# Optimization experiments

Measured on AMD Instinct MI355X. Metric: run time of the kernel, lower is better.

## Reference

```python
import jax, jax.numpy as jnp
import numpy as np

N_TOKENS = 16384
D_MODEL = 1024
N_EXPERTS = 4
TOP_K = 2
LN_EPS = 1e-6


def setup_inputs() -> dict:
    key = jax.random.key(0)
    ks = jax.random.split(key, 6)
    d, e = D_MODEL, N_EXPERTS
    return {
        "x": jax.random.normal(ks[0], (N_TOKENS, d), jnp.float32),
        "gate_w": jax.random.normal(ks[1], (e, d), jnp.float32) * (1.0 / np.sqrt(d)),
        "w1": jax.random.normal(ks[2], (e, 2 * d, d), jnp.float32) * (1.0 / np.sqrt(d)),
        "b1": jax.random.normal(ks[3], (e, 2 * d), jnp.float32) * 0.01,
        "w2": jax.random.normal(ks[4], (e, d, 2 * d), jnp.float32) * (1.0 / np.sqrt(2 * d)),
        "b2": jax.random.normal(ks[5], (e, d), jnp.float32) * 0.01,
        "gamma": jnp.ones((e, d), jnp.float32),
        "beta": jnp.zeros((e, d), jnp.float32),
    }


def _expert_ffn(x, w1e, b1e, w2e, b2e, ge, be):
    h = jax.nn.gelu(x @ w1e.T + b1e, approximate=False)   # [N, 2d]
    z = x + (h @ w2e.T + b2e)                              # residual, [N, d]
    mu = jnp.mean(z, axis=-1, keepdims=True)
    var = jnp.var(z, axis=-1, keepdims=True)
    return (z - mu) * jax.lax.rsqrt(var + LN_EPS) * ge + be


def reference(x, gate_w, w1, b1, w2, b2, gamma, beta):
    n = x.shape[0]
    scores = x @ gate_w.T                                  # [N, E]
    ew, ei = jax.lax.top_k(scores, TOP_K)                  # [N, K]
    ew = jax.nn.softmax(ew, axis=-1)
    # combine weights: dense [N, E] routing matrix (each row has K nonzeros)
    comb = jnp.zeros_like(scores).at[jnp.arange(n)[:, None], ei].add(ew)
    y = jnp.zeros_like(x)
    for e in range(N_EXPERTS):  # small fixed expert count
        y = y + comb[:, e:e + 1] * _expert_ffn(x, w1[e], b1[e], w2[e], b2[e], gamma[e], beta[e])
    return y
```

## Files before the change

kernel.cpp:

```cpp
#include <hip/hip_runtime.h>
#include <hip/hip_bf16.h>
#include <math.h>

#define NT 16384
#define DM 1024
#define NE 4

typedef __attribute__((ext_vector_type(8))) short short8;
typedef __attribute__((ext_vector_type(4))) float f32x4;

#define GLDS(g, l)                                                        \
  __builtin_amdgcn_global_load_lds(                                       \
      (const __attribute__((address_space(1))) void*)(g),                 \
      (__attribute__((address_space(3))) void*)(l), 16, 0, 0)

__device__ __forceinline__ float bf2f(short h) {
    union { unsigned u; float f; } v;
    v.u = ((unsigned)(unsigned short)h) << 16;
    return v.f;
}

__global__ __launch_bounds__(256) void detect_kernel(
    const unsigned int* __restrict__ xw, int* __restrict__ flag)
{
    __shared__ int red[4];
    const int t = threadIdx.x;
    int cnt = 0;
    #pragma unroll 4
    for (int i = 0; i < 64; ++i) {
        unsigned w = xw[t * 64 + i];
        unsigned e0 = (w >> 7) & 0xFFu;
        cnt += (e0 >= 100u && e0 <= 150u) ? 1 : 0;
    }
    #pragma unroll
    for (int o = 32; o > 0; o >>= 1) cnt += __shfl_xor(cnt, o);
    if ((t & 63) == 0) red[t >> 6] = cnt;
    __syncthreads();
    if (t == 0) {
        int tot = red[0] + red[1] + red[2] + red[3];
        *flag = (tot > 8192) ? 1 : 0;
    }
}

__global__ __launch_bounds__(256) void init_kernel(
    int* __restrict__ counts, int* __restrict__ idx)
{
    const int t = blockIdx.x * 256 + threadIdx.x;
    idx[t] = 0;
    if (t < NE) counts[t] = 0;
}

__global__ __launch_bounds__(256) void convert_big_kernel(
    const float* __restrict__ src, short* __restrict__ dst, int n,
    const int* __restrict__ flag)
{
    if (*flag) return;
    const int stride = gridDim.x * blockDim.x;
    const int t0 = blockIdx.x * blockDim.x + threadIdx.x;
    const float4* s = (const float4*)src;
    for (int i = t0; i < n / 4; i += stride) {
        float4 v = s[i];
        __hip_bfloat16 b0 = __float2bfloat16(v.x);
        __hip_bfloat16 b1 = __float2bfloat16(v.y);
        __hip_bfloat16 b2 = __float2bfloat16(v.z);
        __hip_bfloat16 b3 = __float2bfloat16(v.w);
        short4 o;
        o.x = *(short*)&b0; o.y = *(short*)&b1;
        o.z = *(short*)&b2; o.w = *(short*)&b3;
        *(short4*)(dst + (size_t)i * 4) = o;
    }
}

__global__ __launch_bounds__(256) void convert_small_kernel(
    const void* __restrict__ b1, const void* __restrict__ b2,
    const void* __restrict__ ga, const void* __restrict__ be,
    short* __restrict__ b1d, short* __restrict__ b2d,
    short* __restrict__ gad, short* __restrict__ bed,
    const int* __restrict__ flag)
{
    const int isbf = *flag;
    const int t = blockIdx.x * 256 + threadIdx.x;
    const void* src; short* dst; int i;
    if (t < 8192)      { src = b1; dst = b1d; i = t; }
    else if (t < 12288){ src = b2; dst = b2d; i = t - 8192; }
    else if (t < 16384){ src = ga; dst = gad; i = t - 12288; }
    else               { src = be; dst = bed; i = t - 16384; }
    short v;
    if (isbf) v = ((const short*)src)[i];
    else {
        __hip_bfloat16 b = __float2bfloat16(((const float*)src)[i]);
        v = *(short*)&b;
    }
    dst[i] = v;
}

__global__ __launch_bounds__(256) void gate_kernel(
    const void* __restrict__ x, const void* __restrict__ gw,
    float* __restrict__ comb, int* __restrict__ choice,
    const int* __restrict__ flag)
{
    const int lane  = threadIdx.x & 63;
    const int token = blockIdx.x * 4 + (threadIdx.x >> 6);
    double s0 = 0., s1 = 0., s2 = 0., s3 = 0.;
    if (*flag) {
        const short8* xr = (const short8*)((const short*)x + (size_t)token * DM);
        const short8* g0 = (const short8*)((const short*)gw + 0 * DM);
        const short8* g1 = (const short8*)((const short*)gw + 1 * DM);
        const short8* g2 = (const short8*)((const short*)gw + 2 * DM);
        const short8* g3 = (const short8*)((const short*)gw + 3 * DM);
        #pragma unroll
        for (int c = 0; c < 2; ++c) {
            short8 xv = xr[c * 64 + lane];
            short8 a0 = g0[c * 64 + lane], a1 = g1[c * 64 + lane];
            short8 a2 = g2[c * 64 + lane], a3 = g3[c * 64 + lane];
            #pragma unroll
            for (int j = 0; j < 8; ++j) {
                double xd = (double)bf2f(xv[j]);
                s0 += xd * (double)bf2f(a0[j]);
                s1 += xd * (double)bf2f(a1[j]);
                s2 += xd * (double)bf2f(a2[j]);
                s3 += xd * (double)bf2f(a3[j]);
            }
        }
    } else {
        const float4* xr = (const float4*)((const float*)x + (size_t)token * DM);
        const float4* g0 = (const float4*)((const float*)gw + 0 * DM);
        const float4* g1 = (const float4*)((const float*)gw + 1 * DM);
        const float4* g2 = (const float4*)((const float*)gw + 2 * DM);
        const float4* g3 = (const float4*)((const float*)gw + 3 * DM);
        #pragma unroll
        for (int c = 0; c < 4; ++c) {
            float4 xv = xr[c * 64 + lane];
            float4 a0 = g0[c * 64 + lane], a1 = g1[c * 64 + lane];
            float4 a2 = g2[c * 64 + lane], a3 = g3[c * 64 + lane];
            s0 += (double)xv.x * a0.x + (double)xv.y * a0.y + (double)xv.z * a0.z + (double)xv.w * a0.w;
            s1 += (double)xv.x * a1.x + (double)xv.y * a1.y + (double)xv.z * a1.z + (double)xv.w * a1.w;
            s2 += (double)xv.x * a2.x + (double)xv.y * a2.y + (double)xv.z * a2.z + (double)xv.w * a2.w;
            s3 += (double)xv.x * a3.x + (double)xv.y * a3.y + (double)xv.z * a3.z + (double)xv.w * a3.w;
        }
    }
    #pragma unroll
    for (int off = 32; off > 0; off >>= 1) {
        s0 += __shfl_xor(s0, off);
        s1 += __shfl_xor(s1, off);
        s2 += __shfl_xor(s2, off);
        s3 += __shfl_xor(s3, off);
    }
    if (lane == 0) {
        double s[4] = {s0, s1, s2, s3};
        int i1 = 0;
        #pragma unroll
        for (int e = 1; e < 4; ++e) if (s[e] > s[i1]) i1 = e;
        int i2 = -1;
        #pragma unroll
        for (int e = 0; e < 4; ++e) {
            if (e == i1) continue;
            if (i2 < 0 || s[e] > s[i2]) i2 = e;
        }
        float e2 = expf((float)(s[i2] - s[i1]));
        float wa = 1.0f / (1.0f + e2);
        float wb = e2 * wa;
        float* cr = comb + (size_t)token * 4;
        #pragma unroll
        for (int e = 0; e < 4; ++e)
            cr[e] = (e == i1) ? wa : ((e == i2) ? wb : 0.0f);
        choice[token] = i1 | (i2 << 8);
    }
}

__global__ __launch_bounds__(256) void route_kernel(
    const int* __restrict__ choice, int* __restrict__ counts,
    int* __restrict__ idx, int* __restrict__ pos)
{
    __shared__ int T[4][8];
    __shared__ int base[4];
    const int tid = threadIdx.x, w = tid >> 6, lane = tid & 63;
    const int t = blockIdx.x * 256 + tid;
    const int c = choice[t];
    const int e0 = c & 0xFF, e1 = (c >> 8) & 0xFF;
    const unsigned long long lt = ((unsigned long long)1 << lane) - 1;
    int rank0 = 0, rank1 = 0;
    #pragma unroll
    for (int e = 0; e < 4; ++e) {
        unsigned long long m0 = __ballot(e0 == e);
        unsigned long long m1 = __ballot(e1 == e);
        if (e0 == e) rank0 = __popcll(m0 & lt);
        if (e1 == e) rank1 = __popcll(m1 & lt);
        if (lane == 0) { T[w][e] = __popcll(m0); T[w][4 + e] = __popcll(m1); }
    }
    __syncthreads();
    if (tid < 4) {
        int tot = 0;
        #pragma unroll
        for (int w2 = 0; w2 < 4; ++w2) tot += T[w2][tid] + T[w2][4 + tid];
        base[tid] = atomicAdd(&counts[tid], tot);
    }
    __syncthreads();
    int off0 = base[e0], off1 = base[e1];
    #pragma unroll
    for (int w2 = 0; w2 < 4; ++w2) {
        if (w2 < w) off0 += T[w2][e0];
        off1 += T[w2][e1];
        if (w2 < w) off1 += T[w2][4 + e1];
    }
    const int p0 = off0 + rank0;
    const int p1 = off1 + rank1;
    idx[e0 * NT + p0] = t;
    idx[e1 * NT + p1] = t;
    pos[t] = p0 | (p1 << 16);
}

template <int EPI, int BM, int BN>
__global__ __launch_bounds__(512, 2) void gemm256(
    const short* __restrict__ Araw, const short* __restrict__ Acvt,
    const short* __restrict__ Braw, const short* __restrict__ Bcvt,
    const short* __restrict__ biasAll,
    void* __restrict__ Cout,
    const int* __restrict__ idxAll,
    const int* __restrict__ counts,
    int c0, int N, int K, const int* __restrict__ flag,
    int eArg, int Rarg)
{
    constexpr int WM = 2, WN = 4;
    constexpr int WTM = BM / WM;
    constexpr int WTN = BN / WN;
    constexpr int MT  = WTM / 16;
    constexpr int NTt = WTN / 16;
    constexpr int ACH = BM / 64;
    constexpr int BCH = BN / 64;
    constexpr int NLD = ACH + BCH;

    const int e    = (Rarg < 0) ? eArg : (int)blockIdx.z;
    const int cnt  = counts[e] - c0;
    const int rowc = (int)blockIdx.y * BM;
    if (rowc >= cnt) return;

    int hRow0 = 0, zRow0 = 0;
    if (Rarg >= 0) {
        hRow0 = e * Rarg;
        int pre = 0;
        #pragma unroll
        for (int i = 0; i < NE; ++i) pre += (i < e) ? counts[i] : 0;
        zRow0 = pre + c0;
    }

    const short* A = (*flag) ? Araw : Acvt;
    const short* B = ((*flag) ? Braw : Bcvt) + (size_t)e * 2 * DM * DM;
    const short* bias = biasAll + (size_t)e * N;

    __shared__ __align__(16) short sA[2][BM * 64];
    __shared__ __align__(16) short sB[2][BN * 64];

    const int tid  = threadIdx.x;
    const int wid  = tid >> 6;
    const int col0 = (int)blockIdx.x * BN;
    const int wm = wid >> 2, wn = wid & 3;
    const int quad = (tid & 63) >> 4;
    const int mrow = tid & 15;

    const int scol = (((tid & 7) ^ ((tid >> 3) & 7)) * 8);
    const short* gA[ACH];
    const short* gB[BCH];
    #pragma unroll
    for (int i = 0; i < ACH; ++i) {
        const int lr = i * 64 + (tid >> 3);
        size_t grow;
        if (EPI == 0) grow = (size_t)idxAll[(size_t)e * NT + c0 + rowc + lr];
        else          grow = (size_t)(hRow0 + rowc + lr);
        gA[i] = A + grow * (size_t)K + scol;
    }
    #pragma unroll
    for (int j = 0; j < BCH; ++j)
        gB[j] = B + (size_t)(col0 + j * 64 + (tid >> 3)) * K + scol;

    f32x4 acc[MT][NTt];
    #pragma unroll
    for (int m = 0; m < MT; ++m)
        #pragma unroll
        for (int n = 0; n < NTt; ++n)
            acc[m][n] = (f32x4){0.f, 0.f, 0.f, 0.f};

    auto stage = [&](int buf, int k0) {
        short* dA = &sA[buf][0] + wid * 512;
        short* dB = &sB[buf][0] + wid * 512;
        #pragma unroll
        for (int i = 0; i < ACH; ++i) GLDS(gA[i] + k0, dA + i * 4096);
        #pragma unroll
        for (int j = 0; j < BCH; ++j) GLDS(gB[j] + k0, dB + j * 4096);
    };

    const int swz  = (mrow & 7) << 4;
    const int boff = (quad * 16) ^ swz;

    const int ntiles = K / 64;
    stage(0, 0);
    int cur = 0;
    for (int t = 0; t < ntiles; ++t) {
        if (t + 1 < ntiles) {
            stage(cur ^ 1, (t + 1) * 64);
            if (NLD == 8)
                asm volatile("s_waitcnt vmcnt(8)" ::: "memory");
            else
                asm volatile("s_waitcnt vmcnt(6)" ::: "memory");
        } else {
            asm volatile("s_waitcnt vmcnt(0)" ::: "memory");
        }
        __builtin_amdgcn_s_barrier();
        __builtin_amdgcn_sched_barrier(0);
        const char* sAc = (const char*)&sA[cur][0];
        const char* sBc = (const char*)&sB[cur][0];
        #pragma unroll
        for (int kk = 0; kk < 64; kk += 32) {
            const int kb = (kk * 2) ^ boff;
            short8 a[MT], b[NTt];
            #pragma unroll
            for (int m = 0; m < MT; ++m) {
                const int R = wm * WTM + m * 16 + mrow;
                a[m] = *(const short8*)(sAc + R * 128 + kb);
            }
            #pragma unroll
            for (int n = 0; n < NTt; ++n) {
                const int R = wn * WTN + n * 16 + mrow;
                b[n] = *(const short8*)(sBc + R * 128 + kb);
            }
            #pragma unroll
            for (int m = 0; m < MT; ++m)
                #pragma unroll
                for (int n = 0; n < NTt; ++n)
                    acc[m][n] = __builtin_amdgcn_mfma_f32_16x16x32_bf16(
                        a[m], b[n], acc[m][n], 0, 0, 0);
        }
        asm volatile("s_waitcnt lgkmcnt(0)" ::: "memory");
        __builtin_amdgcn_sched_barrier(0);
        __builtin_amdgcn_s_barrier();
        cur ^= 1;
    }

    #pragma unroll
    for (int m = 0; m < MT; ++m) {
        #pragma unroll
        for (int n = 0; n < NTt; ++n) {
            const int col = col0 + wn * WTN + n * 16 + mrow;
            const float bval = bf2f(bias[col]);
            #pragma unroll
            for (int i = 0; i < 4; ++i) {
                const int lrow = rowc + wm * WTM + m * 16 + quad * 4 + i;
                if (lrow < cnt) {
                    float v = acc[m][n][i] + bval;
                    if (EPI == 0) {
                        v = 0.5f * v * (1.0f + erff(v * 0.70710678118654752f));
                        ((__hip_bfloat16*)Cout)[(size_t)(hRow0 + lrow) * N + col] =
                            __float2bfloat16(v);
                    } else {
                        ((float*)Cout)[(size_t)(zRow0 + lrow) * N + col] = v;
                    }
                }
            }
        }
    }
}

__global__ __launch_bounds__(256) void ln_fused_kernel(
    const float* __restrict__ z,
    const void* __restrict__ xraw,
    const float* __restrict__ comb,
    const int* __restrict__ choice,
    const int* __restrict__ pos,
    const short* __restrict__ gammaAll,
    const short* __restrict__ betaAll,
    void* __restrict__ y,
    const int* __restrict__ counts, const int* __restrict__ flag)
{
    const int isbf = *flag;
    const int lane = threadIdx.x & 63;
    const int t = blockIdx.x * 4 + (threadIdx.x >> 6);

    const int ca = counts[0], cb = counts[1], cc = counts[2];
    const int ch = choice[t];
    const int e0 = ch & 0xFF, e1 = (ch >> 8) & 0xFF;
    const int pp = pos[t];
    const int p0 = pp & 0xFFFF, p1 = (pp >> 16) & 0xFFFF;
    const int b0r = (e0 > 0 ? ca : 0) + (e0 > 1 ? cb : 0) + (e0 > 2 ? cc : 0);
    const int b1r = (e1 > 0 ? ca : 0) + (e1 > 1 ? cb : 0) + (e1 > 2 ? cc : 0);
    const float w0 = comb[(size_t)t * 4 + e0];
    const float w1 = comb[(size_t)t * 4 + e1];

    const f32x4* z0r = (const f32x4*)(z + (size_t)(b0r + p0) * DM);
    const f32x4* z1r = (const f32x4*)(z + (size_t)(b1r + p1) * DM);

    f32x4 v0[4], v1[4];
    float s0 = 0.f, q0 = 0.f, s1 = 0.f, q1 = 0.f;
    #pragma unroll
    for (int c = 0; c < 4; ++c) {
        f32x4 a = z0r[c * 64 + lane];
        f32x4 b = z1r[c * 64 + lane];
        float xf[4];
        if (isbf) {
            short4 xv = *(const short4*)((const short*)xraw + (size_t)t * DM + c * 256 + lane * 4);
            xf[0] = bf2f(xv.x); xf[1] = bf2f(xv.y); xf[2] = bf2f(xv.z); xf[3] = bf2f(xv.w);
        } else {
            float4 xv = *(const float4*)((const float*)xraw + (size_t)t * DM + c * 256 + lane * 4);
            xf[0] = xv.x; xf[1] = xv.y; xf[2] = xv.z; xf[3] = xv.w;
        }
        #pragma unroll
        for (int j = 0; j < 4; ++j) {
            v0[c][j] = a[j] + xf[j];
            v1[c][j] = b[j] + xf[j];
            s0 += v0[c][j]; q0 += v0[c][j] * v0[c][j];
            s1 += v1[c][j]; q1 += v1[c][j] * v1[c][j];
        }
    }
    #pragma unroll
    for (int o = 32; o > 0; o >>= 1) {
        s0 += __shfl_xor(s0, o); q0 += __shfl_xor(q0, o);
        s1 += __shfl_xor(s1, o); q1 += __shfl_xor(q1, o);
    }
    const float mu0 = s0 * (1.0f / DM);
    const float r0  = rsqrtf(fmaxf(q0 * (1.0f / DM) - mu0 * mu0, 0.0f) + 1e-6f);
    const float mu1 = s1 * (1.0f / DM);
    const float r1  = rsqrtf(fmaxf(q1 * (1.0f / DM) - mu1 * mu1, 0.0f) + 1e-6f);

    #pragma unroll
    for (int c = 0; c < 4; ++c) {
        const int id = c * 256 + lane * 4;
        short4 g0v  = *(const short4*)(gammaAll + (size_t)e0 * DM + id);
        short4 be0v = *(const short4*)(betaAll  + (size_t)e0 * DM + id);
        short4 g1v  = *(const short4*)(gammaAll + (size_t)e1 * DM + id);
        short4 be1v = *(const short4*)(betaAll  + (size_t)e1 * DM + id);
        const float g0f[4]  = {bf2f(g0v.x),  bf2f(g0v.y),  bf2f(g0v.z),  bf2f(g0v.w)};
        const float b0f[4]  = {bf2f(be0v.x), bf2f(be0v.y), bf2f(be0v.z), bf2f(be0v.w)};
        const float g1f[4]  = {bf2f(g1v.x),  bf2f(g1v.y),  bf2f(g1v.z),  bf2f(g1v.w)};
        const float b1f[4]  = {bf2f(be1v.x), bf2f(be1v.y), bf2f(be1v.z), bf2f(be1v.w)};
        float o[4];
        #pragma unroll
        for (int j = 0; j < 4; ++j)
            o[j] = w0 * ((v0[c][j] - mu0) * r0 * g0f[j] + b0f[j])
                 + w1 * ((v1[c][j] - mu1) * r1 * g1f[j] + b1f[j]);
        if (isbf) {
            short4 ov;
            __hip_bfloat16 t0 = __float2bfloat16(o[0]); ov.x = *(short*)&t0;
            __hip_bfloat16 t1 = __float2bfloat16(o[1]); ov.y = *(short*)&t1;
            __hip_bfloat16 t2 = __float2bfloat16(o[2]); ov.z = *(short*)&t2;
            __hip_bfloat16 t3 = __float2bfloat16(o[3]); ov.w = *(short*)&t3;
            *(short4*)((short*)y + (size_t)t * DM + id) = ov;
        } else {
            float4 ov = {o[0], o[1], o[2], o[3]};
            *(float4*)((float*)y + (size_t)t * DM + id) = ov;
        }
    }
}

__global__ __launch_bounds__(256) void ln_kernel(
    const float* __restrict__ z, const void* __restrict__ xraw,
    const float* __restrict__ comb, const int* __restrict__ choice,
    const __hip_bfloat16* __restrict__ gamma,
    const __hip_bfloat16* __restrict__ beta,
    void* __restrict__ y, const int* __restrict__ idxl,
    const int* __restrict__ count, int c0,
    int expert, const int* __restrict__ flag)
{
    const int isbf = *flag;
    const int lane = threadIdx.x & 63;
    const int l    = blockIdx.x * 4 + (threadIdx.x >> 6);
    const int cnt  = *count - c0;
    if (l >= cnt) return;
    const int token = idxl[c0 + l];
    const int ch = choice[token];
    const int e0 = ch & 0xFF, e1 = (ch >> 8) & 0xFF;
    const int firstexp = e0 < e1 ? e0 : e1;
    const int accumulate = (expert != firstexp);

    const f32x4* zr = (const f32x4*)(z + (size_t)l * DM);
    f32x4 v[4];
    float sum = 0.f, ssq = 0.f;
    #pragma unroll
    for (int c = 0; c < 4; ++c) {
        f32x4 zv = zr[c * 64 + lane];
        if (isbf) {
            short4 xv = *(const short4*)((const short*)xraw + (size_t)token * DM + c * 256 + lane * 4);
            v[c][0] = zv[0] + bf2f(xv.x);
            v[c][1] = zv[1] + bf2f(xv.y);
            v[c][2] = zv[2] + bf2f(xv.z);
            v[c][3] = zv[3] + bf2f(xv.w);
        } else {
            float4 xv = *(const float4*)((const float*)xraw + (size_t)token * DM + c * 256 + lane * 4);
            v[c][0] = zv[0] + xv.x;
            v[c][1] = zv[1] + xv.y;
            v[c][2] = zv[2] + xv.z;
            v[c][3] = zv[3] + xv.w;
        }
        #pragma unroll
        for (int j = 0; j < 4; ++j) { sum += v[c][j]; ssq += v[c][j] * v[c][j]; }
    }
    #pragma unroll
    for (int off = 32; off > 0; off >>= 1) {
        sum += __shfl_xor(sum, off);
        ssq += __shfl_xor(ssq, off);
    }
    const float mu   = sum * (1.0f / DM);
    const float var  = fmaxf(ssq * (1.0f / DM) - mu * mu, 0.0f);
    const float rstd = rsqrtf(var + 1e-6f);
    const float w    = comb[(size_t)token * 4 + expert];
    #pragma unroll
    for (int c = 0; c < 4; ++c) {
        #pragma unroll
        for (int j = 0; j < 4; ++j) {
            const int id = c * 256 + lane * 4 + j;
            const float g = __bfloat162float(gamma[id]);
            const float b = __bfloat162float(beta[id]);
            float o = w * ((v[c][j] - mu) * rstd * g + b);
            if (isbf) {
                __hip_bfloat16* yr = (__hip_bfloat16*)y + (size_t)token * DM;
                if (accumulate) o += __bfloat162float(yr[id]);
                yr[id] = __float2bfloat16(o);
            } else {
                float* yr = (float*)y + (size_t)token * DM;
                if (accumulate) o += yr[id];
                yr[id] = o;
            }
        }
    }
}

extern "C" void kernel_launch(void* const* d_in, const int* in_sizes, int n_in,
                              void* d_out, int out_size, void* d_ws, size_t ws_size,
                              hipStream_t stream)
{
    char* ws = (char*)d_ws;
    size_t off = 0;
    auto alloc = [&](size_t bytes) -> char* {
        char* p = ws + off;
        off = (off + bytes + 255) & ~(size_t)255;
        return p;
    };
    int*   flag   = (int*)  alloc(256);
    float* comb   = (float*)alloc((size_t)NT * 4 * sizeof(float));
    int*   choice = (int*)  alloc((size_t)NT * sizeof(int));
    int*   counts = (int*)  alloc(NE * sizeof(int));
    int*   idx    = (int*)  alloc((size_t)NE * NT * sizeof(int));
    int*   pos    = (int*)  alloc((size_t)NT * sizeof(int));
    short* b1b    = (short*)alloc((size_t)NE * 2 * DM * 2);
    short* b2b    = (short*)alloc((size_t)NE * DM * 2);
    short* gb     = (short*)alloc((size_t)NE * DM * 2);
    short* bb     = (short*)alloc((size_t)NE * DM * 2);
    short* w1b    = (short*)alloc((size_t)NE * 2 * DM * DM * 2);
    short* w2b    = (short*)alloc((size_t)NE * 2 * DM * DM * 2);
    short* xb     = (short*)alloc((size_t)NT * DM * 2);
    const size_t fixed = off;

    detect_kernel<<<1, 256, 0, stream>>>((const unsigned int*)d_in[0], flag);
    init_kernel<<<(NE * NT) / 256, 256, 0, stream>>>(counts, idx);

    convert_big_kernel<<<2048, 256, 0, stream>>>((const float*)d_in[0], xb,
                                                 NT * DM, flag);
    convert_big_kernel<<<2048, 256, 0, stream>>>((const float*)d_in[2], w1b,
                                                 NE * 2 * DM * DM, flag);
    convert_big_kernel<<<2048, 256, 0, stream>>>((const float*)d_in[4], w2b,
                                                 NE * 2 * DM * DM, flag);
    convert_small_kernel<<<80, 256, 0, stream>>>(d_in[3], d_in[5], d_in[6], d_in[7],
                                                 b1b, b2b, gb, bb, flag);

    gate_kernel<<<NT / 4, 256, 0, stream>>>(d_in[0], d_in[1], comb, choice, flag);
    route_kernel<<<NT / 256, 256, 0, stream>>>(choice, counts, idx, pos);

    const size_t zBytes = (size_t)2 * NT * DM * sizeof(float);
    int R = 0;
    for (int cand = 2048; cand >= 1024; cand >>= 1) {
        const size_t hBytes = (size_t)NE * cand * 2 * DM * 2;
        if (fixed + hBytes + zBytes + 4096 <= ws_size) { R = cand; break; }
    }

    if (R > 0) {
        short* h = (short*)alloc((size_t)NE * R * 2 * DM * 2);
        float* z = (float*)alloc(zBytes);
        for (int c0 = 0; c0 < NT; c0 += R) {
            dim3 g1(2 * DM / 256, R / 256, NE);
            gemm256<0, 256, 256><<<g1, 512, 0, stream>>>(
                (const short*)d_in[0], xb, (const short*)d_in[2], w1b, b1b,
                (void*)h, idx, counts, c0, 2 * DM, DM, flag, 0, R);
            dim3 g2(DM / 256, R / 128, NE);
            gemm256<1, 128, 256><<<g2, 512, 0, stream>>>(
                h, h, (const short*)d_in[4], w2b, b2b,
                (void*)z, idx, counts, c0, DM, 2 * DM, flag, 0, R);
        }
        ln_fused_kernel<<<NT / 4, 256, 0, stream>>>(z, d_in[0], comb, choice, pos,
                                                    gb, bb, d_out, counts, flag);
    } else {
        int cap = NT;
        while (cap > 512 && fixed + (size_t)cap * 8192 > ws_size) cap >>= 1;
        short* h = (short*)alloc((size_t)cap * 2 * DM * 2);
        float* z = (float*)alloc((size_t)cap * DM * sizeof(float));
        for (int e = 0; e < NE; ++e) {
            for (int c0 = 0; c0 < NT; c0 += cap) {
                dim3 g1(2 * DM / 256, cap / 256, 1);
                gemm256<0, 256, 256><<<g1, 512, 0, stream>>>(
                    (const short*)d_in[0], xb, (const short*)d_in[2], w1b, b1b,
                    (void*)h, idx, counts, c0, 2 * DM, DM, flag, e, -1);
                dim3 g2(DM / 256, cap / 128, 1);
                gemm256<1, 128, 256><<<g2, 512, 0, stream>>>(
                    h, h, (const short*)d_in[4], w2b, b2b,
                    (void*)z, idx, counts, c0, DM, 2 * DM, flag, e, -1);
                ln_kernel<<<cap / 4, 256, 0, stream>>>(z, d_in[0], comb, choice,
                    (const __hip_bfloat16*)(gb + (size_t)e * DM),
                    (const __hip_bfloat16*)(bb + (size_t)e * DM),
                    d_out, idx + (size_t)e * NT, counts + e, c0, e, flag);
            }
        }
    }
}
```

Before: 793.1 us.

## Restructure expert GEMMs into phased pipeline with XCD-aware block remapping

Replaces the double-buffered GEMM main loop with a per-k-tile schedule of four phases. Each phase loads a quarter of the LDS fragments, issues part of the next tile's global-to-LDS loads, raises wave priority around the MFMA burst, and synchronises with barriers, so loads overlap compute at finer grain. The second GEMM changes from 128x256 to 256x128 tiles. For the 8x8x4 grid, block IDs are remapped so blocks of the same expert and row band land on the same XCD, which should improve L2 reuse. The cost is more barriers per tile and hand-tuned vmcnt counts that must match the staging order exactly.

After: 818.5 us. 3.2% more time.

```diff
diff --git a/kernel.cpp b/kernel.cpp
--- a/kernel.cpp
+++ b/kernel.cpp
@@ -210,8 +210,8 @@
     pos[t] = p0 | (p1 << 16);
 }
 
-template <int EPI, int BM, int BN>
-__global__ __launch_bounds__(512, 2) void gemm256(
+template <int EPI, int BN>
+__global__ __launch_bounds__(512, 2) void gemm8p(
     const short* __restrict__ Araw, const short* __restrict__ Acvt,
     const short* __restrict__ Braw, const short* __restrict__ Bcvt,
     const short* __restrict__ biasAll,
@@ -221,18 +221,27 @@
     int c0, int N, int K, const int* __restrict__ flag,
     int eArg, int Rarg)
 {
-    constexpr int WM = 2, WN = 4;
-    constexpr int WTM = BM / WM;
-    constexpr int WTN = BN / WN;
-    constexpr int MT  = WTM / 16;
+    constexpr int BM  = 256;
+    constexpr int WTM = 128;
+    constexpr int WTN = BN / 4;
+    constexpr int MT  = 8;
     constexpr int NTt = WTN / 16;
-    constexpr int ACH = BM / 64;
+    constexpr int NPH = NTt / 2;
+    constexpr int ACH = 4;
     constexpr int BCH = BN / 64;
-    constexpr int NLD = ACH + BCH;
-
-    const int e    = (Rarg < 0) ? eArg : (int)blockIdx.z;
+
+    int bx = (int)blockIdx.x, by = (int)blockIdx.y, bz = (int)blockIdx.z;
+    if (Rarg >= 0 && gridDim.x == 8 && gridDim.y == 8 && gridDim.z == 4) {
+        const int lid  = bx + 8 * by + 64 * bz;
+        const int xcd  = lid & 7, slot = lid >> 3;
+        bz = xcd >> 1;
+        by = (xcd & 1) * 4 + (slot >> 3);
+        bx = slot & 7;
+    }
+
+    const int e    = (Rarg < 0) ? eArg : bz;
     const int cnt  = counts[e] - c0;
-    const int rowc = (int)blockIdx.y * BM;
+    const int rowc = by * BM;
     if (rowc >= cnt) return;
 
     int hRow0 = 0, zRow0 = 0;
@@ -253,7 +262,7 @@
 
     const int tid  = threadIdx.x;
     const int wid  = tid >> 6;
-    const int col0 = (int)blockIdx.x * BN;
+    const int col0 = bx * BN;
     const int wm = wid >> 2, wn = wid & 3;
     const int quad = (tid & 63) >> 4;
     const int mrow = tid & 15;
@@ -280,61 +289,86 @@
         for (int n = 0; n < NTt; ++n)
             acc[m][n] = (f32x4){0.f, 0.f, 0.f, 0.f};
 
-    auto stage = [&](int buf, int k0) {
-        short* dA = &sA[buf][0] + wid * 512;
-        short* dB = &sB[buf][0] + wid * 512;
-        #pragma unroll
-        for (int i = 0; i < ACH; ++i) GLDS(gA[i] + k0, dA + i * 4096);
-        #pragma unroll
-        for (int j = 0; j < BCH; ++j) GLDS(gB[j] + k0, dB + j * 4096);
+    auto stA = [&](int bp, int u, int k0) {
+        GLDS(gA[u] + k0, &sA[bp][u * 4096] + wid * 512);
     };
-
-    const int swz  = (mrow & 7) << 4;
-    const int boff = (quad * 16) ^ swz;
-
+    auto stB = [&](int bp, int u, int k0) {
+        GLDS(gB[u] + k0, &sB[bp][u * 4096] + wid * 512);
+    };
+
+    const int boff = (quad * 16) ^ ((mrow & 7) << 4);
     const int ntiles = K / 64;
-    stage(0, 0);
-    int cur = 0;
-    for (int t = 0; t < ntiles; ++t) {
-        if (t + 1 < ntiles) {
-            stage(cur ^ 1, (t + 1) * 64);
-            if (NLD == 8)
-                asm volatile("s_waitcnt vmcnt(8)" ::: "memory");
-            else
-                asm volatile("s_waitcnt vmcnt(6)" ::: "memory");
+
+    #pragma unroll
+    for (int u = 0; u < ACH; ++u) stA(0, u, 0);
+    #pragma unroll
+    for (int u = 0; u < BCH; ++u) stB(0, u, 0);
+    if (ntiles > 1) {
+        stA(1, 0, 64); stA(1, 2, 64);
+        asm volatile("s_waitcnt vmcnt(2)" ::: "memory");
+    } else {
+        asm volatile("s_waitcnt vmcnt(0)" ::: "memory");
+    }
+    __builtin_amdgcn_sched_barrier(0);
+    __builtin_amdgcn_s_barrier();
+
+#define PHASE(MH, NH, ISSUE, VMOP)                                             \
+    {                                                                          \
+        short8 pa[4][2]; short8 pb[NPH][2];                                    \
+        const char* sAc = (const char*)&sA[p][0];                              \
+        const char* sBc = (const char*)&sB[p][0];                              \
+        _Pragma("unroll")                                                      \
+        for (int m = 0; m < 4; ++m) {                                          \
+            const int Rr = wm * WTM + ((MH) * 4 + m) * 16 + mrow;              \
+            pa[m][0] = *(const short8*)(sAc + Rr * 128 + (0 ^ boff));          \
+            pa[m][1] = *(const short8*)(sAc + Rr * 128 + (64 ^ boff));         \
+        }                                                                      \
+        _Pragma("unroll")                                                      \
+        for (int n = 0; n < NPH; ++n) {                                        \
+            const int Rr = wn * WTN + ((NH) * NPH + n) * 16 + mrow;            \
+            pb[n][0] = *(const short8*)(sBc + Rr * 128 + (0 ^ boff));          \
+            pb[n][1] = *(const short8*)(sBc + Rr * 128 + (64 ^ boff));         \
+        }                                                                      \
+        ISSUE                                                                  \
+        __builtin_amdgcn_sched_barrier(0);                                     \
+        __builtin_amdgcn_s_barrier();                                          \
+        __builtin_amdgcn_s_setprio(1);                                         \
+        _Pragma("unroll")                                                      \
+        for (int m = 0; m < 4; ++m)                                            \
+            _Pragma("unroll")                                                  \
+            for (int n = 0; n < NPH; ++n) {                                    \
+                acc[(MH)*4+m][(NH)*NPH+n] =                                    \
+                    __builtin_amdgcn_mfma_f32_16x16x32_bf16(                   \
+                        pa[m][0], pb[n][0], acc[(MH)*4+m][(NH)*NPH+n], 0,0,0); \
+                acc[(MH)*4+m][(NH)*NPH+n] =                                    \
+                    __builtin_amdgcn_mfma_f32_16x16x32_bf16(                   \
+                        pa[m][1], pb[n][1], acc[(MH)*4+m][(NH)*NPH+n], 0,0,0); \
+            }                                                                  \
+        __builtin_amdgcn_s_setprio(0);                                         \
+        VMOP                                                                   \
+        __builtin_amdgcn_sched_barrier(0);                                     \
+        __builtin_amdgcn_s_barrier();                                          \
+    }
+
+    int p = 0;
+    for (int kt = 0; kt < ntiles; ++kt, p ^= 1) {
+        const int k1 = (kt + 1) * 64, k2 = (kt + 2) * 64;
+        const bool h1 = (kt + 1 < ntiles), h2 = (kt + 2 < ntiles);
+        PHASE(0, 0, if (h1) { stA(p ^ 1, 1, k1); stA(p ^ 1, 3, k1); }, )
+        PHASE(0, 1, if (h1) { stB(p ^ 1, 0, k1); stB(p ^ 1, 1, k1); }, )
+        if constexpr (BCH == 4) {
+            PHASE(1, 0, if (h1) { stB(p ^ 1, 2, k1); stB(p ^ 1, 3, k1); }, )
+            PHASE(1, 1, if (h2) { stA(p, 0, k2); stA(p, 2, k2); },
+                  if (h2)      { asm volatile("s_waitcnt vmcnt(2)" ::: "memory"); }
+                  else if (h1) { asm volatile("s_waitcnt vmcnt(0)" ::: "memory"); })
         } else {
-            asm volatile("s_waitcnt vmcnt(0)" ::: "memory");
-        }
-        __builtin_amdgcn_s_barrier();
-        __builtin_amdgcn_sched_barrier(0);
-        const char* sAc = (const char*)&sA[cur][0];
-        const char* sBc = (const char*)&sB[cur][0];
-        #pragma unroll
-        for (int kk = 0; kk < 64; kk += 32) {
-            const int kb = (kk * 2) ^ boff;
-            short8 a[MT], b[NTt];
-            #pragma unroll
-            for (int m = 0; m < MT; ++m) {
-                const int R = wm * WTM + m * 16 + mrow;
-                a[m] = *(const short8*)(sAc + R * 128 + kb);
-            }
-            #pragma unroll
-            for (int n = 0; n < NTt; ++n) {
-                const int R = wn * WTN + n * 16 + mrow;
-                b[n] = *(const short8*)(sBc + R * 128 + kb);
-            }
-            #pragma unroll
-            for (int m = 0; m < MT; ++m)
-                #pragma unroll
-                for (int n = 0; n < NTt; ++n)
-                    acc[m][n] = __builtin_amdgcn_mfma_f32_16x16x32_bf16(
-                        a[m], b[n], acc[m][n], 0, 0, 0);
-        }
-        asm volatile("s_waitcnt lgkmcnt(0)" ::: "memory");
-        __builtin_amdgcn_sched_barrier(0);
-        __builtin_amdgcn_s_barrier();
-        cur ^= 1;
-    }
+            PHASE(1, 0, if (h2) { stA(p, 0, k2); stA(p, 2, k2); }, )
+            PHASE(1, 1, ,
+                  if (h2)      { asm volatile("s_waitcnt vmcnt(2)" ::: "memory"); }
+                  else if (h1) { asm volatile("s_waitcnt vmcnt(0)" ::: "memory"); })
+        }
+    }
+#undef PHASE
 
     #pragma unroll
     for (int m = 0; m < MT; ++m) {
@@ -575,11 +609,11 @@
         float* z = (float*)alloc(zBytes);
         for (int c0 = 0; c0 < NT; c0 += R) {
             dim3 g1(2 * DM / 256, R / 256, NE);
-            gemm256<0, 256, 256><<<g1, 512, 0, stream>>>(
+            gemm8p<0, 256><<<g1, 512, 0, stream>>>(
                 (const short*)d_in[0], xb, (const short*)d_in[2], w1b, b1b,
                 (void*)h, idx, counts, c0, 2 * DM, DM, flag, 0, R);
-            dim3 g2(DM / 256, R / 128, NE);
-            gemm256<1, 128, 256><<<g2, 512, 0, stream>>>(
+            dim3 g2(DM / 128, R / 256, NE);
+            gemm8p<1, 128><<<g2, 512, 0, stream>>>(
                 h, h, (const short*)d_in[4], w2b, b2b,
                 (void*)z, idx, counts, c0, DM, 2 * DM, flag, 0, R);
         }
@@ -593,11 +627,11 @@
         for (int e = 0; e < NE; ++e) {
             for (int c0 = 0; c0 < NT; c0 += cap) {
                 dim3 g1(2 * DM / 256, cap / 256, 1);
-                gemm256<0, 256, 256><<<g1, 512, 0, stream>>>(
+                gemm8p<0, 256><<<g1, 512, 0, stream>>>(
                     (const short*)d_in[0], xb, (const short*)d_in[2], w1b, b1b,
                     (void*)h, idx, counts, c0, 2 * DM, DM, flag, e, -1);
-                dim3 g2(DM / 256, cap / 128, 1);
-                gemm256<1, 128, 256><<<g2, 512, 0, stream>>>(
+                dim3 g2(DM / 128, cap / 256, 1);
+                gemm8p<1, 128><<<g2, 512, 0, stream>>>(
                     h, h, (const short*)d_in[4], w2b, b2b,
                     (void*)z, idx, counts, c0, DM, 2 * DM, flag, e, -1);
                 ln_kernel<<<cap / 4, 256, 0, stream>>>(z, d_in[0], comb, choice,
```
